# Kernel optimization log

Measured on AMD Instinct MI355X. Metric: run time of the kernel, lower is better.

Reference implementation:

```python
import jax, jax.numpy as jnp
import numpy as np

B, T, D, H = 4, 2048, 1024, 16
HD = D // H
EPS = 1e-5
NEG = 1e10


def setup_inputs() -> dict:
    key = jax.random.key(0)
    k1, k2, k3 = jax.random.split(key, 3)
    return {
        "target": jax.random.normal(k1, (B, T, D), dtype=jnp.float32),
        "w_qkv": jax.random.normal(k2, (D, 3 * D), dtype=jnp.float32) * 0.02,
        "w_proj": jax.random.normal(k3, (D, D), dtype=jnp.float32) * (0.02 / np.sqrt(24.0)),
        "b_proj": jnp.zeros((D,), dtype=jnp.float32),
        "ln_gamma": jnp.ones((D,), dtype=jnp.float32),
        "ln_beta": jnp.zeros((D,), dtype=jnp.float32),
    }


def reference(target, w_qkv, w_proj, b_proj, ln_gamma, ln_beta):
    b, t, d = target.shape
    resid = target
    qkv = target @ w_qkv                      # [B,T,3D]
    q, k, v = jnp.split(qkv, 3, axis=-1)
    # [B,H,T,hd]
    q = q.reshape(b, t, H, HD).transpose(0, 2, 1, 3)
    k = k.reshape(b, t, H, HD).transpose(0, 2, 1, 3)
    v = v.reshape(b, t, H, HD).transpose(0, 2, 1, 3)
    scores = jnp.einsum("bhqd,bhkd->bhqk", q, k) * (1.0 / np.sqrt(HD))
    causal = (jnp.arange(t)[:, None] >= jnp.arange(t)[None, :]).astype(scores.dtype)
    scores = scores * causal - (1.0 - causal) * NEG
    attn = jax.nn.softmax(scores, axis=-1)
    out = jnp.einsum("bhqk,bhkd->bhqd", attn, v)
    out = out.transpose(0, 2, 1, 3).reshape(b, t, d)
    proj = out @ w_proj + b_proj
    x = proj + resid
    mu = jnp.mean(x, axis=-1, keepdims=True)
    var = jnp.var(x, axis=-1, keepdims=True)
    return ((x - mu) * jax.lax.rsqrt(var + EPS)) * ln_gamma + ln_beta
```

## Files before the change

### kernel.cpp

```cpp
#include <hip/hip_runtime.h>
#include <hip/hip_bf16.h>

#define Bsz 4
#define Tseq 2048
#define Dmodel 1024
#define Hn 16
#define HD 64
#define EPS 1e-5f
#define QSCALE 0.18033688011112042f

typedef __attribute__((ext_vector_type(8))) short bf16x8;
typedef __attribute__((ext_vector_type(4))) short bf16x4;
typedef __attribute__((ext_vector_type(4))) float f32x4;
typedef __attribute__((ext_vector_type(4))) unsigned short us4;
typedef __attribute__((ext_vector_type(2))) unsigned uint2v;

typedef const __attribute__((address_space(1))) void* gas_t;
typedef __attribute__((address_space(3))) void* las_t;

__device__ __forceinline__ unsigned short f2bf(float x) {
    unsigned u = __builtin_bit_cast(unsigned, x);
    u += 0x7fffu + ((u >> 16) & 1u);
    return (unsigned short)(u >> 16);
}
__device__ __forceinline__ unsigned pack2bf_t(float a, float b) {
    return __builtin_amdgcn_perm(__builtin_bit_cast(unsigned, b),
                                 __builtin_bit_cast(unsigned, a), 0x07060302u);
}

__device__ __forceinline__ float exp2_raw(float x) {
#if __has_builtin(__builtin_amdgcn_exp2f)
    return __builtin_amdgcn_exp2f(x);
#else
    float r;
    asm("v_exp_f32 %0, %1" : "=v"(r) : "v"(x));
    return r;
#endif
}

__device__ __forceinline__ f32x4 mfma16x16x16(bf16x4 a, bf16x4 b, f32x4 c) {
#if __has_builtin(__builtin_amdgcn_mfma_f32_16x16x16bf16_1k)
    return __builtin_amdgcn_mfma_f32_16x16x16bf16_1k(a, b, c, 0, 0, 0);
#else
    asm("v_mfma_f32_16x16x16_bf16 %0, %1, %2, %0" : "+v"(c) : "v"(a), "v"(b));
    return c;
#endif
}

__global__ void cast_bf16(const float* __restrict__ in, unsigned short* __restrict__ out) {
    int i = (blockIdx.x * 256 + threadIdx.x) * 4;
    float4 v = *(const float4*)(in + i);
    us4 o = { f2bf(v.x), f2bf(v.y), f2bf(v.z), f2bf(v.w) };
    *(us4*)(out + i) = o;
}

__global__ void transpose_cast(const float* __restrict__ in, unsigned short* __restrict__ out,
                               int K, int N) {
    __shared__ unsigned short t[32][33];
    int k0 = blockIdx.y * 32, n0 = blockIdx.x * 32;
    int tx = threadIdx.x, ty = threadIdx.y;
    #pragma unroll
    for (int i = 0; i < 32; i += 8)
        t[ty + i][tx] = f2bf(in[(size_t)(k0 + ty + i) * N + n0 + tx]);
    __syncthreads();
    #pragma unroll
    for (int i = 0; i < 32; i += 8)
        out[(size_t)(n0 + ty + i) * K + k0 + tx] = t[tx][ty + i];
}

template<bool OUT_BF16, bool SCALEQ>
__global__ __launch_bounds__(256)
void gemm_mfma(const unsigned short* __restrict__ A,
               const unsigned short* __restrict__ Bt,
               void* __restrict__ Cv, int M, int N, int K,
               const float* __restrict__ bias, const float* __restrict__ resid) {
    __shared__ unsigned short As[2][128 * 32];
    __shared__ unsigned short Bs[2][128 * 32];
    const int tid = threadIdx.x;
    const int w = tid >> 6, lane = tid & 63;
    const int l16 = lane & 15, quad = lane >> 4;

    const int lin = blockIdx.y * gridDim.x + blockIdx.x;
    const int chunk = (gridDim.x * gridDim.y) >> 3;
    const int neff = (lin & 7) * chunk + (lin >> 3);
    const int bx = neff % gridDim.x, by = neff / gridDim.x;
    const int m0 = by * 128, n0 = bx * 128;

    f32x4 acc[4][4];
    #pragma unroll
    for (int i = 0; i < 4; ++i)
        #pragma unroll
        for (int j = 0; j < 4; ++j)
            acc[i][j] = f32x4{0.f, 0.f, 0.f, 0.f};

    const int lrow = lane >> 2, lcol = lane & 3;
    const unsigned short* ag = A  + (size_t)(m0 + w * 32 + lrow) * K + lcol * 8;
    const unsigned short* bg = Bt + (size_t)(n0 + w * 32 + lrow) * K + lcol * 8;
    unsigned short* al0 = As[0] + (w * 32) * 32;
    unsigned short* al1 = As[0] + (w * 32 + 16) * 32;
    unsigned short* ah0 = As[1] + (w * 32) * 32;
    unsigned short* ah1 = As[1] + (w * 32 + 16) * 32;
    unsigned short* bl0 = Bs[0] + (w * 32) * 32;
    unsigned short* bl1 = Bs[0] + (w * 32 + 16) * 32;
    unsigned short* bh0 = Bs[1] + (w * 32) * 32;
    unsigned short* bh1 = Bs[1] + (w * 32 + 16) * 32;
    const int am = (w >> 1) * 64, bn = (w & 1) * 64;

    for (int k0 = 0; k0 < K; k0 += 64) {
        __builtin_amdgcn_global_load_lds((gas_t)(ag + k0),               (las_t)al0, 16, 0, 0);
        __builtin_amdgcn_global_load_lds((gas_t)(ag + 16 * K + k0),      (las_t)al1, 16, 0, 0);
        __builtin_amdgcn_global_load_lds((gas_t)(ag + k0 + 32),          (las_t)ah0, 16, 0, 0);
        __builtin_amdgcn_global_load_lds((gas_t)(ag + 16 * K + k0 + 32), (las_t)ah1, 16, 0, 0);
        __builtin_amdgcn_global_load_lds((gas_t)(bg + k0),               (las_t)bl0, 16, 0, 0);
        __builtin_amdgcn_global_load_lds((gas_t)(bg + 16 * K + k0),      (las_t)bl1, 16, 0, 0);
        __builtin_amdgcn_global_load_lds((gas_t)(bg + k0 + 32),          (las_t)bh0, 16, 0, 0);
        __builtin_amdgcn_global_load_lds((gas_t)(bg + 16 * K + k0 + 32), (las_t)bh1, 16, 0, 0);
        __syncthreads();

        #pragma unroll
        for (int ks = 0; ks < 2; ++ks) {
            bf16x8 af[4], bf[4];
            #pragma unroll
            for (int i = 0; i < 4; ++i)
                af[i] = *(const bf16x8*)&As[ks][(am + i * 16 + l16) * 32 + quad * 8];
            #pragma unroll
            for (int j = 0; j < 4; ++j)
                bf[j] = *(const bf16x8*)&Bs[ks][(bn + j * 16 + l16) * 32 + quad * 8];
            #pragma unroll
            for (int i = 0; i < 4; ++i)
                #pragma unroll
                for (int j = 0; j < 4; ++j)
                    acc[i][j] = __builtin_amdgcn_mfma_f32_16x16x32_bf16(af[i], bf[j], acc[i][j], 0, 0, 0);
        }
        __syncthreads();
    }

    #pragma unroll
    for (int i = 0; i < 4; ++i) {
        #pragma unroll
        for (int j = 0; j < 4; ++j) {
            const int col = n0 + bn + j * 16 + l16;
            const float scale = (SCALEQ && col < Dmodel) ? QSCALE : 1.0f;
            #pragma unroll
            for (int r = 0; r < 4; ++r) {
                const int row = m0 + am + i * 16 + quad * 4 + r;
                if (OUT_BF16) {
                    ((unsigned short*)Cv)[(size_t)row * N + col] = f2bf(acc[i][j][r] * scale);
                } else {
                    float v = acc[i][j][r] + bias[col] + resid[(size_t)row * N + col];
                    ((float*)Cv)[(size_t)row * N + col] = v;
                }
            }
        }
    }
}

__global__ __launch_bounds__(256)
void flash_attn(const unsigned short* __restrict__ qkv, unsigned short* __restrict__ out) {
    const int lin = blockIdx.y * gridDim.x + blockIdx.x;
    const int xcd = lin & 7, local = lin >> 3;
    const int bh = xcd + 8 * (local & 7);
    const int x = local >> 3;
    const int qt_lo = x, qt_hi = (Tseq / 64 - 1) - x;
    const int h = bh & (Hn - 1), b = bh >> 4;
    const int tid = threadIdx.x;
    const int wave = tid >> 6;
    const int lane = tid & 63;
    const int l16 = lane & 15;
    const int quad = lane >> 4;

    __shared__ unsigned short Ks[2][2][64 * 32];
    __shared__ unsigned short Vs[2][64 * 64];

    const unsigned short* qrow = qkv + ((size_t)(b * Tseq + wave * 16 + l16)) * 3072 + h * HD;
    const unsigned short* qhi = qrow + (size_t)qt_hi * 64 * 3072;
    const unsigned short* qlo = qrow + (size_t)qt_lo * 64 * 3072;
    bf16x8 qh0 = *(const bf16x8*)(qhi + quad * 8);
    bf16x8 qh1 = *(const bf16x8*)(qhi + 32 + quad * 8);
    bf16x8 ql0 = *(const bf16x8*)(qlo + quad * 8);
    bf16x8 ql1 = *(const bf16x8*)(qlo + 32 + quad * 8);

    float l_hi = 0.f, l_lo = 0.f;
    f32x4 ohi[4], olo[4];
    #pragma unroll
    for (int nt = 0; nt < 4; ++nt) {
        ohi[nt] = f32x4{0.f, 0.f, 0.f, 0.f};
        olo[nt] = f32x4{0.f, 0.f, 0.f, 0.f};
    }

    unsigned vrb[4];
    #pragma unroll
    for (int ntd = 0; ntd < 4; ++ntd) {
        const int d = ntd * 16 + l16;
        const int X = (d + (d >> 3)) & 7;
        vrb[ntd] = (unsigned)(d * 128 + (quad & 1) * 8)
                 ^ (unsigned)(X << 4) ^ (unsigned)((quad >> 1) << 4);
    }

    const unsigned short* kbase = qkv + (size_t)b * Tseq * 3072 + Dmodel + h * HD;
    const unsigned short* vbase = kbase + Dmodel;
    const unsigned short* kg = kbase + (size_t)(wave * 16 + (lane >> 2)) * 3072 + (lane & 3) * 8;
    const int vp = tid >> 3, vc = tid & 7;
    const unsigned short* vsrc = vbase + (size_t)(2 * vp) * 3072 + vc * 8;

    auto stageK = [&](int buf, size_t koff) {
        __builtin_amdgcn_global_load_lds((gas_t)(kg + koff),
                                         (las_t)&Ks[buf][0][wave * 16 * 32], 16, 0, 0);
        __builtin_amdgcn_global_load_lds((gas_t)(kg + koff + 32),
                                         (las_t)&Ks[buf][1][wave * 16 * 32], 16, 0, 0);
    };
    auto writeV = [&](int buf, const bf16x8& va, const bf16x8& vb) {
        const int kc = vp >> 2;
        const int kin = (2 * vp) & 7;
        #pragma unroll
        for (int j = 0; j < 8; ++j) {
            const int d = vc * 8 + j;
            const int pc = kc ^ ((d + (d >> 3)) & 7);
            unsigned pk = (unsigned)(unsigned short)va[j]
                        | ((unsigned)(unsigned short)vb[j] << 16);
            *(unsigned*)&Vs[buf][d * 64 + pc * 8 + kin] = pk;
        }
    };

    auto compute = [&](int buf, int q0t, const bf16x8& qf0, const bf16x8& qf1,
                       f32x4* oacc, float& l_part, bool diag, int k0g) {
        __builtin_amdgcn_s_setprio(1);
        f32x4 st[4];
        #pragma unroll
        for (int nt = 0; nt < 4; ++nt) {
            f32x4 a = {0.f, 0.f, 0.f, 0.f};
            bf16x8 kf0 = *(const bf16x8*)&Ks[buf][0][(nt * 16 + l16) * 32 + quad * 8];
            a = __builtin_amdgcn_mfma_f32_16x16x32_bf16(kf0, qf0, a, 0, 0, 0);
            bf16x8 kf1 = *(const bf16x8*)&Ks[buf][1][(nt * 16 + l16) * 32 + quad * 8];
            a = __builtin_amdgcn_mfma_f32_16x16x32_bf16(kf1, qf1, a, 0, 0, 0);
            st[nt] = a;
        }
        if (diag) {
            const int qg = q0t + wave * 16 + l16;
            #pragma unroll
            for (int nt = 0; nt < 4; ++nt) {
                const int kgl = k0g + nt * 16 + quad * 4;
                #pragma unroll
                for (int r = 0; r < 4; ++r)
                    if (kgl + r > qg) st[nt][r] = -1e30f;
            }
        }
        bf16x4 pa[4];
        #pragma unroll
        for (int nt = 0; nt < 4; ++nt) {
            float p0 = exp2_raw(st[nt][0]);
            float p1 = exp2_raw(st[nt][1]);
            float p2 = exp2_raw(st[nt][2]);
            float p3 = exp2_raw(st[nt][3]);
            l_part += (p0 + p1) + (p2 + p3);
            uint2v t;
            t.x = pack2bf_t(p0, p1);
            t.y = pack2bf_t(p2, p3);
            pa[nt] = __builtin_bit_cast(bf16x4, t);
        }
        const char* vsb = (const char*)&Vs[buf][0];
        #pragma unroll
        for (int ntk = 0; ntk < 4; ++ntk) {
            #pragma unroll
            for (int ntd = 0; ntd < 4; ++ntd) {
                bf16x4 vf = *(const bf16x4*)(vsb + (vrb[ntd] ^ (unsigned)(ntk << 5)));
                oacc[ntd] = mfma16x16x16(pa[ntk], vf, oacc[ntd]);
            }
        }
        __builtin_amdgcn_s_setprio(0);
    };

    stageK(0, 0);
    bf16x8 va = *(const bf16x8*)(vsrc);
    bf16x8 vb = *(const bf16x8*)(vsrc + 3072);
    writeV(0, va, vb);
    __syncthreads();

    int cur = 0;
    for (int kt = 0; kt <= qt_hi; ++kt) {
        if (kt < qt_hi) {
            const size_t koff_n = (size_t)(kt + 1) * 64 * 3072;
            stageK(cur ^ 1, koff_n);
            va = *(const bf16x8*)(vsrc + koff_n);
            vb = *(const bf16x8*)(vsrc + koff_n + 3072);
        }

        compute(cur, qt_hi * 64, qh0, qh1, ohi, l_hi, kt == qt_hi, kt * 64);
        if (kt <= qt_lo)
            compute(cur, qt_lo * 64, ql0, ql1, olo, l_lo, kt == qt_lo, kt * 64);

        if (kt < qt_hi) writeV(cur ^ 1, va, vb);
        __syncthreads();
        cur ^= 1;
    }

    auto epilogue = [&](int q0t, f32x4* oacc, float l_part) {
        l_part += __shfl_xor(l_part, 16, 64);
        l_part += __shfl_xor(l_part, 32, 64);
        float inv[4];
        #pragma unroll
        for (int r = 0; r < 4; ++r) {
            float lr = __shfl(l_part, quad * 4 + r, 64);
            inv[r] = __builtin_amdgcn_rcpf(lr);
        }
        unsigned short* obase =
            out + ((size_t)(b * Tseq + q0t + wave * 16)) * Dmodel + h * HD;
        #pragma unroll
        for (int nt = 0; nt < 4; ++nt) {
            #pragma unroll
            for (int r = 0; r < 4; ++r) {
                int row = quad * 4 + r;
                obase[(size_t)row * Dmodel + nt * 16 + l16] = f2bf(oacc[nt][r] * inv[r]);
            }
        }
    };
    epilogue(qt_hi * 64, ohi, l_hi);
    epilogue(qt_lo * 64, olo, l_lo);
}

__global__ void ln_kernel(float* __restrict__ x, const float* __restrict__ gamma,
                          const float* __restrict__ beta) {
    const int row = blockIdx.x;
    float* xr = x + (size_t)row * Dmodel;
    const int tid = threadIdx.x;
    __shared__ float rs[256], rs2[256];

    float4 v = *(const float4*)(xr + tid * 4);
    float s  = v.x + v.y + v.z + v.w;
    float s2 = v.x * v.x + v.y * v.y + v.z * v.z + v.w * v.w;
    rs[tid] = s; rs2[tid] = s2;
    __syncthreads();
    for (int off = 128; off; off >>= 1) {
        if (tid < off) { rs[tid] += rs[tid + off]; rs2[tid] += rs2[tid + off]; }
        __syncthreads();
    }
    const float mu  = rs[0] * (1.0f / Dmodel);
    const float var = rs2[0] * (1.0f / Dmodel) - mu * mu;
    const float rstd = rsqrtf(var + EPS);

    float4 g = *(const float4*)(gamma + tid * 4);
    float4 bt = *(const float4*)(beta + tid * 4);
    float4 o;
    o.x = (v.x - mu) * rstd * g.x + bt.x;
    o.y = (v.y - mu) * rstd * g.y + bt.y;
    o.z = (v.z - mu) * rstd * g.z + bt.z;
    o.w = (v.w - mu) * rstd * g.w + bt.w;
    *(float4*)(xr + tid * 4) = o;
}

extern "C" void kernel_launch(void* const* d_in, const int* in_sizes, int n_in,
                              void* d_out, int out_size, void* d_ws, size_t ws_size,
                              hipStream_t stream) {
    const float* target   = (const float*)d_in[0];
    const float* w_qkv    = (const float*)d_in[1];
    const float* w_proj   = (const float*)d_in[2];
    const float* b_proj   = (const float*)d_in[3];
    const float* ln_gamma = (const float*)d_in[4];
    const float* ln_beta  = (const float*)d_in[5];
    float* out = (float*)d_out;

    const int M = Bsz * Tseq;

    char* ws = (char*)d_ws;
    unsigned short* qkv_bf16 = (unsigned short*)(ws);
    unsigned short* attn_bf  = (unsigned short*)(ws + 48ull * 1024 * 1024);
    unsigned short* tgt_bf   = (unsigned short*)(ws + 64ull * 1024 * 1024);
    unsigned short* wqT      = (unsigned short*)(ws + 80ull * 1024 * 1024);
    unsigned short* wpT      = (unsigned short*)(ws + 86ull * 1024 * 1024);

    cast_bf16<<<dim3(M * Dmodel / 1024), 256, 0, stream>>>(target, tgt_bf);
    transpose_cast<<<dim3(3072 / 32, Dmodel / 32), dim3(32, 8), 0, stream>>>(
        w_qkv, wqT, Dmodel, 3072);
    transpose_cast<<<dim3(Dmodel / 32, Dmodel / 32), dim3(32, 8), 0, stream>>>(
        w_proj, wpT, Dmodel, Dmodel);

    gemm_mfma<true, true><<<dim3(3072 / 128, M / 128), 256, 0, stream>>>(
        tgt_bf, wqT, qkv_bf16, M, 3072, Dmodel, nullptr, nullptr);

    flash_attn<<<dim3(16, Bsz * Hn), 256, 0, stream>>>(qkv_bf16, attn_bf);

    gemm_mfma<false, false><<<dim3(Dmodel / 128, M / 128), 256, 0, stream>>>(
        attn_bf, wpT, out, M, Dmodel, Dmodel, b_proj, target);

    ln_kernel<<<dim3(M), 256, 0, stream>>>(out, ln_gamma, ln_beta);
}
```

Baseline: 272.3 us.

## Merge prep kernels, compute softmax row sums via MFMA, shuffle-reduce LayerNorm

The three preprocessing kernels (activation cast and two weight transpose-casts) become one launch that dispatches on block index, saving two launches. In flash attention, the per-lane scalar row-sum adds and the shuffle reduction in the epilogue are replaced by an extra MFMA of P against a ones vector, which yields row sums already laid out per row. The LayerNorm reduction moves from a shared-memory tree with many barriers to wave shuffles plus one barrier. The row sums are now taken from bf16-rounded P, which matches the numerator, and each tile adds four MFMAs.

Measured after the change: 273.5 us. No clear change (+0.5%).

```diff
diff --git a/kernel.cpp b/kernel.cpp
--- a/kernel.cpp
+++ b/kernel.cpp
@@ -47,25 +47,41 @@
 #endif
 }
 
-__global__ void cast_bf16(const float* __restrict__ in, unsigned short* __restrict__ out) {
-    int i = (blockIdx.x * 256 + threadIdx.x) * 4;
-    float4 v = *(const float4*)(in + i);
-    us4 o = { f2bf(v.x), f2bf(v.y), f2bf(v.z), f2bf(v.w) };
-    *(us4*)(out + i) = o;
-}
-
-__global__ void transpose_cast(const float* __restrict__ in, unsigned short* __restrict__ out,
-                               int K, int N) {
+__global__ __launch_bounds__(256)
+void prep(const float* __restrict__ target, unsigned short* __restrict__ tgt_bf,
+          const float* __restrict__ w_qkv, unsigned short* __restrict__ wqT,
+          const float* __restrict__ w_proj, unsigned short* __restrict__ wpT) {
+    const int bid = blockIdx.x;
+    const int tid = threadIdx.x;
+    if (bid < 8192) {
+        int i = (bid * 256 + tid) * 4;
+        float4 v = *(const float4*)(target + i);
+        us4 o = { f2bf(v.x), f2bf(v.y), f2bf(v.z), f2bf(v.w) };
+        *(us4*)(tgt_bf + i) = o;
+        return;
+    }
     __shared__ unsigned short t[32][33];
-    int k0 = blockIdx.y * 32, n0 = blockIdx.x * 32;
-    int tx = threadIdx.x, ty = threadIdx.y;
+    const float* in;
+    unsigned short* outp;
+    int K = 1024, N, bx, by;
+    if (bid < 8192 + 3072) {
+        const int b2 = bid - 8192;
+        in = w_qkv; outp = wqT; N = 3072;
+        bx = b2 % 96; by = b2 / 96;
+    } else {
+        const int b3 = bid - 8192 - 3072;
+        in = w_proj; outp = wpT; N = 1024;
+        bx = b3 & 31; by = b3 >> 5;
+    }
+    const int k0 = by * 32, n0 = bx * 32;
+    const int tx = tid & 31, ty = tid >> 5;
     #pragma unroll
     for (int i = 0; i < 32; i += 8)
         t[ty + i][tx] = f2bf(in[(size_t)(k0 + ty + i) * N + n0 + tx]);
     __syncthreads();
     #pragma unroll
     for (int i = 0; i < 32; i += 8)
-        out[(size_t)(n0 + ty + i) * K + k0 + tx] = t[tx][ty + i];
+        outp[(size_t)(n0 + ty + i) * K + k0 + tx] = t[tx][ty + i];
 }
 
 template<bool OUT_BF16, bool SCALEQ>
@@ -180,13 +196,14 @@
     bf16x8 ql0 = *(const bf16x8*)(qlo + quad * 8);
     bf16x8 ql1 = *(const bf16x8*)(qlo + 32 + quad * 8);
 
-    float l_hi = 0.f, l_lo = 0.f;
+    f32x4 lacc_hi = {0.f, 0.f, 0.f, 0.f}, lacc_lo = {0.f, 0.f, 0.f, 0.f};
     f32x4 ohi[4], olo[4];
     #pragma unroll
     for (int nt = 0; nt < 4; ++nt) {
         ohi[nt] = f32x4{0.f, 0.f, 0.f, 0.f};
         olo[nt] = f32x4{0.f, 0.f, 0.f, 0.f};
     }
+    const bf16x4 vones = { (short)0x3F80, (short)0x3F80, (short)0x3F80, (short)0x3F80 };
 
     unsigned vrb[4];
     #pragma unroll
@@ -223,7 +240,7 @@
     };
 
     auto compute = [&](int buf, int q0t, const bf16x8& qf0, const bf16x8& qf1,
-                       f32x4* oacc, float& l_part, bool diag, int k0g) {
+                       f32x4* oacc, f32x4& lacc, bool diag, int k0g) {
         __builtin_amdgcn_s_setprio(1);
         f32x4 st[4];
         #pragma unroll
@@ -252,7 +269,6 @@
             float p1 = exp2_raw(st[nt][1]);
             float p2 = exp2_raw(st[nt][2]);
             float p3 = exp2_raw(st[nt][3]);
-            l_part += (p0 + p1) + (p2 + p3);
             uint2v t;
             t.x = pack2bf_t(p0, p1);
             t.y = pack2bf_t(p2, p3);
@@ -261,6 +277,7 @@
         const char* vsb = (const char*)&Vs[buf][0];
         #pragma unroll
         for (int ntk = 0; ntk < 4; ++ntk) {
+            lacc = mfma16x16x16(pa[ntk], vones, lacc);
             #pragma unroll
             for (int ntd = 0; ntd < 4; ++ntd) {
                 bf16x4 vf = *(const bf16x4*)(vsb + (vrb[ntd] ^ (unsigned)(ntk << 5)));
@@ -285,24 +302,20 @@
             vb = *(const bf16x8*)(vsrc + koff_n + 3072);
         }
 
-        compute(cur, qt_hi * 64, qh0, qh1, ohi, l_hi, kt == qt_hi, kt * 64);
+        compute(cur, qt_hi * 64, qh0, qh1, ohi, lacc_hi, kt == qt_hi, kt * 64);
         if (kt <= qt_lo)
-            compute(cur, qt_lo * 64, ql0, ql1, olo, l_lo, kt == qt_lo, kt * 64);
+            compute(cur, qt_lo * 64, ql0, ql1, olo, lacc_lo, kt == qt_lo, kt * 64);
 
         if (kt < qt_hi) writeV(cur ^ 1, va, vb);
         __syncthreads();
         cur ^= 1;
     }
 
-    auto epilogue = [&](int q0t, f32x4* oacc, float l_part) {
-        l_part += __shfl_xor(l_part, 16, 64);
-        l_part += __shfl_xor(l_part, 32, 64);
+    auto epilogue = [&](int q0t, f32x4* oacc, const f32x4& lacc) {
         float inv[4];
         #pragma unroll
-        for (int r = 0; r < 4; ++r) {
-            float lr = __shfl(l_part, quad * 4 + r, 64);
-            inv[r] = __builtin_amdgcn_rcpf(lr);
-        }
+        for (int r = 0; r < 4; ++r)
+            inv[r] = __builtin_amdgcn_rcpf(lacc[r]);
         unsigned short* obase =
             out + ((size_t)(b * Tseq + q0t + wave * 16)) * Dmodel + h * HD;
         #pragma unroll
@@ -314,28 +327,34 @@
             }
         }
     };
-    epilogue(qt_hi * 64, ohi, l_hi);
-    epilogue(qt_lo * 64, olo, l_lo);
-}
-
-__global__ void ln_kernel(float* __restrict__ x, const float* __restrict__ gamma,
-                          const float* __restrict__ beta) {
+    epilogue(qt_hi * 64, ohi, lacc_hi);
+    epilogue(qt_lo * 64, olo, lacc_lo);
+}
+
+__global__ __launch_bounds__(256)
+void ln_kernel(float* __restrict__ x, const float* __restrict__ gamma,
+               const float* __restrict__ beta) {
     const int row = blockIdx.x;
     float* xr = x + (size_t)row * Dmodel;
     const int tid = threadIdx.x;
-    __shared__ float rs[256], rs2[256];
+    const int wave = tid >> 6;
+    __shared__ float ws[4], ws2[4];
 
     float4 v = *(const float4*)(xr + tid * 4);
     float s  = v.x + v.y + v.z + v.w;
     float s2 = v.x * v.x + v.y * v.y + v.z * v.z + v.w * v.w;
-    rs[tid] = s; rs2[tid] = s2;
+    #pragma unroll
+    for (int off = 32; off; off >>= 1) {
+        s  += __shfl_xor(s, off, 64);
+        s2 += __shfl_xor(s2, off, 64);
+    }
+    if ((tid & 63) == 0) { ws[wave] = s; ws2[wave] = s2; }
     __syncthreads();
-    for (int off = 128; off; off >>= 1) {
-        if (tid < off) { rs[tid] += rs[tid + off]; rs2[tid] += rs2[tid + off]; }
-        __syncthreads();
-    }
-    const float mu  = rs[0] * (1.0f / Dmodel);
-    const float var = rs2[0] * (1.0f / Dmodel) - mu * mu;
+    s  = (ws[0] + ws[1]) + (ws[2] + ws[3]);
+    s2 = (ws2[0] + ws2[1]) + (ws2[2] + ws2[3]);
+
+    const float mu  = s * (1.0f / Dmodel);
+    const float var = s2 * (1.0f / Dmodel) - mu * mu;
     const float rstd = rsqrtf(var + EPS);
 
     float4 g = *(const float4*)(gamma + tid * 4);
@@ -368,11 +387,8 @@
     unsigned short* wqT      = (unsigned short*)(ws + 80ull * 1024 * 1024);
     unsigned short* wpT      = (unsigned short*)(ws + 86ull * 1024 * 1024);
 
-    cast_bf16<<<dim3(M * Dmodel / 1024), 256, 0, stream>>>(target, tgt_bf);
-    transpose_cast<<<dim3(3072 / 32, Dmodel / 32), dim3(32, 8), 0, stream>>>(
-        w_qkv, wqT, Dmodel, 3072);
-    transpose_cast<<<dim3(Dmodel / 32, Dmodel / 32), dim3(32, 8), 0, stream>>>(
-        w_proj, wpT, Dmodel, Dmodel);
+    prep<<<dim3(8192 + 3072 + 1024), 256, 0, stream>>>(
+        target, tgt_bf, w_qkv, wqT, w_proj, wpT);
 
     gemm_mfma<true, true><<<dim3(3072 / 128, M / 128), 256, 0, stream>>>(
         tgt_bf, wqT, qkv_bf16, M, 3072, Dmodel, nullptr, nullptr);
```
